# Performance work log

Measured on AMD Instinct MI355X. Metric: run time of the kernel, lower is better.

## Reference

```python
import jax, jax.numpy as jnp
import numpy as np

B, TC, D = 256, 256, 2048


def setup_inputs() -> dict:
    key = jax.random.key(0)
    k1, k2, k3 = jax.random.split(key, 3)
    h_dec = jax.random.normal(k1, (B, D), dtype=jnp.float32)
    prev_h_dec = jax.random.normal(k2, (B, TC, D), dtype=jnp.float32)
    dec_mask = jnp.ones((B, TC), dtype=bool)
    # nn.Bilinear weight [1, D, D] squeezed to [D, D]; torch init scale ~ 1/sqrt(D)
    W = jax.random.normal(k3, (D, D), dtype=jnp.float32) * (1.0 / np.sqrt(D))
    return {"h_dec": h_dec, "prev_h_dec": prev_h_dec, "dec_mask": dec_mask, "W": W}


def reference(h_dec, prev_h_dec, dec_mask, W):
    # Bilinear score: e[b,t] = h_dec[b] @ W @ prev_h_dec[b,t]
    hw = jnp.einsum('bd,de->be', h_dec, W)            # [B, D] dense GEMM
    e = jnp.einsum('be,bte->bt', hw, prev_h_dec)      # [B, TC]
    # masked_fill(~mask, -inf) then amax-stabilized softmax (jax.nn.softmax is max-stabilized)
    e = jnp.where(dec_mask, e, -jnp.inf)
    at_weights = jax.nn.softmax(e, axis=1)            # [B, TC]
    context_dec = jnp.einsum('bt,btd->bd', at_weights, prev_h_dec)  # [B, D]
    new_prev_h_dec = jnp.concatenate([prev_h_dec, h_dec[:, None, :]], axis=1)  # [B, TC+1, D]
    return context_dec, new_prev_h_dec
```

## Files before the change

### kernel.cpp

```cpp
#include <hip/hip_runtime.h>
#include <math.h>

#define BB  256
#define TCC 256
#define DD  2048

typedef float4 f4;

__global__ __launch_bounds__(256) void hw_gemm_partial(
    const float* __restrict__ h,
    const float* __restrict__ W,
    float* __restrict__ part)
{
    __shared__ float hs[32][68];
    __shared__ float wsm[32][64];

    const int tid = threadIdx.x;
    const int e0 = blockIdx.x * 64;
    const int b0 = blockIdx.y * 64;
    const int z  = blockIdx.z;

    float acc[4][4];
    #pragma unroll
    for (int i = 0; i < 4; i++)
        #pragma unroll
        for (int j = 0; j < 4; j++) acc[i][j] = 0.f;

    const int ie = tid & 15;
    const int ib = tid >> 4;

    const int hr = tid >> 2;
    const int hc = (tid & 3) * 8;
    const int wr = tid >> 3;
    const int wc = (tid & 7) * 8;

    for (int d0 = z * 512; d0 < z * 512 + 512; d0 += 32) {
        f4 ha = *(const f4*)&h[(size_t)(b0 + hr) * DD + d0 + hc];
        f4 hb = *(const f4*)&h[(size_t)(b0 + hr) * DD + d0 + hc + 4];
        hs[hc + 0][hr] = ha.x; hs[hc + 1][hr] = ha.y;
        hs[hc + 2][hr] = ha.z; hs[hc + 3][hr] = ha.w;
        hs[hc + 4][hr] = hb.x; hs[hc + 5][hr] = hb.y;
        hs[hc + 6][hr] = hb.z; hs[hc + 7][hr] = hb.w;
        f4 wa = *(const f4*)&W[(size_t)(d0 + wr) * DD + e0 + wc];
        f4 wb = *(const f4*)&W[(size_t)(d0 + wr) * DD + e0 + wc + 4];
        *(f4*)&wsm[wr][wc]     = wa;
        *(f4*)&wsm[wr][wc + 4] = wb;
        __syncthreads();

        #pragma unroll
        for (int dd = 0; dd < 32; dd++) {
            f4 hv = *(const f4*)&hs[dd][ib * 4];
            f4 wv = *(const f4*)&wsm[dd][ie * 4];
            float hvv[4] = {hv.x, hv.y, hv.z, hv.w};
            float wvv[4] = {wv.x, wv.y, wv.z, wv.w};
            #pragma unroll
            for (int i = 0; i < 4; i++)
                #pragma unroll
                for (int j = 0; j < 4; j++)
                    acc[i][j] += hvv[i] * wvv[j];
        }
        __syncthreads();
    }

    #pragma unroll
    for (int i = 0; i < 4; i++) {
        f4 v = make_float4(acc[i][0], acc[i][1], acc[i][2], acc[i][3]);
        *(f4*)&part[((size_t)z * BB + b0 + ib * 4 + i) * DD + e0 + ie * 4] = v;
    }
}

__global__ __launch_bounds__(1024) void attn_fused(
    const float* __restrict__ h_dec,
    const float* __restrict__ prev,
    const unsigned char* __restrict__ maskb,
    const float* __restrict__ part,
    float* __restrict__ out)
{
    __shared__ float hw[DD];
    __shared__ float wred[2][16];
    __shared__ float gm[4], gl[4];

    const int b   = blockIdx.x;
    const int tid = threadIdx.x;

    for (int k = tid; k < DD; k += 1024) {
        hw[k] = part[(size_t)b * DD + k]
              + part[((size_t)BB + b) * DD + k]
              + part[((size_t)2 * BB + b) * DD + k]
              + part[((size_t)3 * BB + b) * DD + k];
    }

    int nz = 0;
    #pragma unroll
    for (int k = 1; k < 64; k++)
        if ((k & 3) != 0) nz += (maskb[k] != 0);
    const bool boolLayout = (nz > 0);
    const int* maski = (const int*)maskb;

    __syncthreads();

    const int g    = tid >> 8;
    const int tl   = tid & 255;
    const int wv   = tid >> 6;
    const int lane = tid & 63;

    float hwr[8];
    #pragma unroll
    for (int j = 0; j < 8; j++) hwr[j] = hw[tl * 8 + j];

    float m = -INFINITY, l = 0.f;
    float acc[8] = {0.f, 0.f, 0.f, 0.f, 0.f, 0.f, 0.f, 0.f};

    const float* pb = prev + (size_t)b * TCC * DD + tl * 8;
    float* cp = out + (size_t)BB * DD + (size_t)b * (TCC + 1) * DD + tl * 8;

    f4 c0 = *(const f4*)(pb + (size_t)(g * 64) * DD);
    f4 c1 = *(const f4*)(pb + (size_t)(g * 64) * DD + 4);

    for (int i = 0; i < 64; i++) {
        const int t = g * 64 + i;
        f4 n0 = c0, n1 = c1;
        if (i < 63) {
            n0 = *(const f4*)(pb + (size_t)(t + 1) * DD);
            n1 = *(const f4*)(pb + (size_t)(t + 1) * DD + 4);
        }
        *(f4*)(cp + (size_t)t * DD)     = c0;
        *(f4*)(cp + (size_t)t * DD + 4) = c1;
        float p = c0.x * hwr[0] + c0.y * hwr[1] + c0.z * hwr[2] + c0.w * hwr[3]
                + c1.x * hwr[4] + c1.y * hwr[5] + c1.z * hwr[6] + c1.w * hwr[7];
        #pragma unroll
        for (int off = 32; off; off >>= 1) p += __shfl_xor(p, off, 64);
        if (lane == 0) wred[i & 1][wv] = p;
        __syncthreads();
        const float e = wred[i & 1][4 * g] + wred[i & 1][4 * g + 1]
                      + wred[i & 1][4 * g + 2] + wred[i & 1][4 * g + 3];
        const bool mk = boolLayout ? (maskb[(size_t)b * TCC + t] != 0)
                                   : (maski[(size_t)b * TCC + t] != 0);
        if (mk) {
            if (e > m) {
                const float sc = __expf(m - e);
                l *= sc;
                #pragma unroll
                for (int j = 0; j < 8; j++) acc[j] *= sc;
                m = e;
            }
            const float w = __expf(e - m);
            l += w;
            acc[0] += w * c0.x; acc[1] += w * c0.y;
            acc[2] += w * c0.z; acc[3] += w * c0.w;
            acc[4] += w * c1.x; acc[5] += w * c1.y;
            acc[6] += w * c1.z; acc[7] += w * c1.w;
        }
        c0 = n0; c1 = n1;
    }

    __syncthreads();
    if (tl == 0) { gm[g] = m; gl[g] = l; }
    __syncthreads();
    const float mstar = fmaxf(fmaxf(gm[0], gm[1]), fmaxf(gm[2], gm[3]));
    float L = 0.f;
    #pragma unroll
    for (int q = 0; q < 4; q++) L += gl[q] * __expf(gm[q] - mstar);
    const float f = __expf(gm[g] - mstar);

    for (int ph = 0; ph < 4; ph++) {
        if (g == ph) {
            #pragma unroll
            for (int j = 0; j < 8; j++) {
                if (ph == 0) hw[tl * 8 + j]  = f * acc[j];
                else         hw[tl * 8 + j] += f * acc[j];
            }
        }
        __syncthreads();
    }

    const float invL = 1.0f / L;
    for (int k = tid; k < DD; k += 1024)
        out[(size_t)b * DD + k] = hw[k] * invL;
    for (int k = tid; k < DD; k += 1024)
        out[(size_t)BB * DD + ((size_t)b * (TCC + 1) + TCC) * DD + k] =
            h_dec[(size_t)b * DD + k];
}

extern "C" void kernel_launch(void* const* d_in, const int* in_sizes, int n_in,
                              void* d_out, int out_size, void* d_ws, size_t ws_size,
                              hipStream_t stream) {
    const float* h_dec = (const float*)d_in[0];
    const float* prev  = (const float*)d_in[1];
    const unsigned char* maskb = (const unsigned char*)d_in[2];
    const float* W = (const float*)d_in[3];
    float* out  = (float*)d_out;
    float* part = (float*)d_ws;

    hipLaunchKernelGGL(hw_gemm_partial, dim3(32, 4, 4), dim3(256), 0, stream,
                       h_dec, W, part);
    hipLaunchKernelGGL(attn_fused, dim3(BB), dim3(1024), 0, stream,
                       h_dec, prev, maskb, part, out);
}
```

Before: 262.8 us.

## Assign whole rows per wavefront to drop per-step block barriers in attention

The attention kernel is restructured so that each of the 16 wavefronts owns 16 full time steps and computes each score with a wavefront-only shuffle reduction. This removes the block-wide __syncthreads and shared-memory reduction that previously ran on every time step. Each wavefront keeps its own online-softmax state, and the 16 partial results are merged serially through a new shared ctx buffer. Loads and stores of prev use nontemporal builtins with 8 independent vector loads in flight per step. In exchange, the explicit next-row prefetch is dropped, the register footprint per thread grows (32 accumulators plus 32 loaded values), and the final merge takes 16 barriered phases instead of 4.

```diff
diff --git a/kernel.cpp b/kernel.cpp
--- a/kernel.cpp
+++ b/kernel.cpp
@@ -6,6 +6,7 @@
 #define DD  2048
 
 typedef float4 f4;
+typedef float __attribute__((ext_vector_type(4))) fv4;
 
 __global__ __launch_bounds__(256) void hw_gemm_partial(
     const float* __restrict__ h,
@@ -69,7 +70,7 @@
     }
 }
 
-__global__ __launch_bounds__(1024) void attn_fused(
+__global__ __launch_bounds__(1024) void attn_fused2(
     const float* __restrict__ h_dec,
     const float* __restrict__ prev,
     const unsigned char* __restrict__ maskb,
@@ -77,8 +78,8 @@
     float* __restrict__ out)
 {
     __shared__ float hw[DD];
-    __shared__ float wred[2][16];
-    __shared__ float gm[4], gl[4];
+    __shared__ float ctx[DD];
+    __shared__ float gm[16], gl[16];
 
     const int b   = blockIdx.x;
     const int tid = threadIdx.x;
@@ -88,6 +89,7 @@
               + part[((size_t)BB + b) * DD + k]
               + part[((size_t)2 * BB + b) * DD + k]
               + part[((size_t)3 * BB + b) * DD + k];
+        ctx[k] = 0.f;
     }
 
     int nz = 0;
@@ -99,76 +101,71 @@
 
     __syncthreads();
 
-    const int g    = tid >> 8;
-    const int tl   = tid & 255;
-    const int wv   = tid >> 6;
-    const int lane = tid & 63;
+    const int w  = tid >> 6;
+    const int ld = tid & 63;
 
-    float hwr[8];
+    const float* pb = prev + (size_t)b * TCC * DD + 4 * ld;
+    float* cp = out + (size_t)BB * DD + (size_t)b * (TCC + 1) * DD + 4 * ld;
+
+    fv4 acc[8];
     #pragma unroll
-    for (int j = 0; j < 8; j++) hwr[j] = hw[tl * 8 + j];
+    for (int j = 0; j < 8; j++) acc[j] = (fv4)(0.f);
+    float m = -INFINITY, l = 0.f;
 
-    float m = -INFINITY, l = 0.f;
-    float acc[8] = {0.f, 0.f, 0.f, 0.f, 0.f, 0.f, 0.f, 0.f};
+    for (int k = 0; k < 16; ++k) {
+        const int t = w * 16 + k;
+        const fv4* src = (const fv4*)(pb + (size_t)t * DD);
+        fv4 v[8];
+        #pragma unroll
+        for (int j = 0; j < 8; ++j) v[j] = __builtin_nontemporal_load(src + 64 * j);
 
-    const float* pb = prev + (size_t)b * TCC * DD + tl * 8;
-    float* cp = out + (size_t)BB * DD + (size_t)b * (TCC + 1) * DD + tl * 8;
+        fv4* dst = (fv4*)(cp + (size_t)t * DD);
+        #pragma unroll
+        for (int j = 0; j < 8; ++j) __builtin_nontemporal_store(v[j], dst + 64 * j);
 
-    f4 c0 = *(const f4*)(pb + (size_t)(g * 64) * DD);
-    f4 c1 = *(const f4*)(pb + (size_t)(g * 64) * DD + 4);
-
-    for (int i = 0; i < 64; i++) {
-        const int t = g * 64 + i;
-        f4 n0 = c0, n1 = c1;
-        if (i < 63) {
-            n0 = *(const f4*)(pb + (size_t)(t + 1) * DD);
-            n1 = *(const f4*)(pb + (size_t)(t + 1) * DD + 4);
+        float p = 0.f;
+        #pragma unroll
+        for (int j = 0; j < 8; ++j) {
+            const fv4 hv = *(const fv4*)&hw[4 * ld + 256 * j];
+            p += v[j].x * hv.x + v[j].y * hv.y + v[j].z * hv.z + v[j].w * hv.w;
         }
-        *(f4*)(cp + (size_t)t * DD)     = c0;
-        *(f4*)(cp + (size_t)t * DD + 4) = c1;
-        float p = c0.x * hwr[0] + c0.y * hwr[1] + c0.z * hwr[2] + c0.w * hwr[3]
-                + c1.x * hwr[4] + c1.y * hwr[5] + c1.z * hwr[6] + c1.w * hwr[7];
         #pragma unroll
         for (int off = 32; off; off >>= 1) p += __shfl_xor(p, off, 64);
-        if (lane == 0) wred[i & 1][wv] = p;
-        __syncthreads();
-        const float e = wred[i & 1][4 * g] + wred[i & 1][4 * g + 1]
-                      + wred[i & 1][4 * g + 2] + wred[i & 1][4 * g + 3];
+
         const bool mk = boolLayout ? (maskb[(size_t)b * TCC + t] != 0)
                                    : (maski[(size_t)b * TCC + t] != 0);
         if (mk) {
-            if (e > m) {
-                const float sc = __expf(m - e);
-                l *= sc;
+            if (p > m) {
+                const float s = __expf(m - p);
+                l *= s;
                 #pragma unroll
-                for (int j = 0; j < 8; j++) acc[j] *= sc;
-                m = e;
+                for (int j = 0; j < 8; j++) acc[j] *= s;
+                m = p;
             }
-            const float w = __expf(e - m);
-            l += w;
-            acc[0] += w * c0.x; acc[1] += w * c0.y;
-            acc[2] += w * c0.z; acc[3] += w * c0.w;
-            acc[4] += w * c1.x; acc[5] += w * c1.y;
-            acc[6] += w * c1.z; acc[7] += w * c1.w;
+            const float wgt = __expf(p - m);
+            l += wgt;
+            #pragma unroll
+            for (int j = 0; j < 8; j++) acc[j] += wgt * v[j];
         }
-        c0 = n0; c1 = n1;
     }
 
+    if (ld == 0) { gm[w] = m; gl[w] = l; }
     __syncthreads();
-    if (tl == 0) { gm[g] = m; gl[g] = l; }
-    __syncthreads();
-    const float mstar = fmaxf(fmaxf(gm[0], gm[1]), fmaxf(gm[2], gm[3]));
+
+    float mstar = -INFINITY;
+    #pragma unroll
+    for (int q = 0; q < 16; q++) mstar = fmaxf(mstar, gm[q]);
     float L = 0.f;
     #pragma unroll
-    for (int q = 0; q < 4; q++) L += gl[q] * __expf(gm[q] - mstar);
-    const float f = __expf(gm[g] - mstar);
+    for (int q = 0; q < 16; q++) L += gl[q] * __expf(gm[q] - mstar);
+    const float f = __expf(m - mstar);
 
-    for (int ph = 0; ph < 4; ph++) {
-        if (g == ph) {
+    for (int ph = 0; ph < 16; ++ph) {
+        if (w == ph) {
             #pragma unroll
-            for (int j = 0; j < 8; j++) {
-                if (ph == 0) hw[tl * 8 + j]  = f * acc[j];
-                else         hw[tl * 8 + j] += f * acc[j];
+            for (int j = 0; j < 8; ++j) {
+                fv4* c = (fv4*)&ctx[4 * ld + 256 * j];
+                *c += f * acc[j];
             }
         }
         __syncthreads();
@@ -176,7 +173,7 @@
 
     const float invL = 1.0f / L;
     for (int k = tid; k < DD; k += 1024)
-        out[(size_t)b * DD + k] = hw[k] * invL;
+        out[(size_t)b * DD + k] = ctx[k] * invL;
     for (int k = tid; k < DD; k += 1024)
         out[(size_t)BB * DD + ((size_t)b * (TCC + 1) + TCC) * DD + k] =
             h_dec[(size_t)b * DD + k];
@@ -194,6 +191,6 @@
 
     hipLaunchKernelGGL(hw_gemm_partial, dim3(32, 4, 4), dim3(256), 0, stream,
                        h_dec, W, part);
-    hipLaunchKernelGGL(attn_fused, dim3(BB), dim3(1024), 0, stream,
+    hipLaunchKernelGGL(attn_fused2, dim3(BB), dim3(1024), 0, stream,
                        h_dec, prev, maskb, part, out);
 }
```

Result: slower. 272.6 us (+3.7%).
